# Kernel tuning notes

Measured on AMD Instinct MI355X. Metric: run time of the kernel, lower is better.

The kernel has to match this reference:

```python
import jax, jax.numpy as jnp
import numpy as np

DIMS = [2048, 2048, 2048, 2048, 1000]
BATCH = 1024
N_RELAX = 25
RELAX_LR = 0.3
N_LAYERS = len(DIMS) - 1  # 4 weight matrices, states indexed 0..4


def setup_inputs() -> dict:
    key = jax.random.key(0)
    ks = jax.random.split(key, N_LAYERS + 1)
    inp = {"x": jax.random.normal(ks[0], (BATCH, DIMS[0]), jnp.float32)}
    for i in range(N_LAYERS):
        scale = np.float32(np.sqrt(2.0 / DIMS[i]))
        inp[f"W{i}"] = jax.random.normal(ks[i + 1], (DIMS[i], DIMS[i + 1]), jnp.float32) * scale
    # biases[0] is never used in forward; biases[1..4] init to zeros as in torch code
    for l in range(1, N_LAYERS + 1):
        inp[f"b{l}"] = jnp.zeros((DIMS[l],), jnp.float32)
    return inp


def _rho(t):
    return jnp.clip(t, 0.0, 1.0)


def _relax(x, Ws, bs):
    # bs[l-1] corresponds to original biases[l] (state l's bias), l = 1..N_LAYERS
    # feedforward initialization pass
    states = [x]
    h = x
    for l in range(N_LAYERS):
        h = _rho(h @ Ws[l] + bs[l])
        states.append(h)

    # Gauss-Seidel sweep: states[l-1] already updated this iteration when l uses it
    def sweep(carry, _):
        full = [x] + list(carry)
        for l in range(1, N_LAYERS + 1):
            ds = -full[l] + bs[l - 1] + _rho(full[l - 1]) @ Ws[l - 1]
            if l < N_LAYERS:
                ds = ds + _rho(full[l + 1]) @ Ws[l].T
            full[l] = _rho(full[l] + RELAX_LR * ds)
        return tuple(full[1:]), None

    carry, _ = jax.lax.scan(sweep, tuple(states[1:]), None, length=N_RELAX)
    return carry


def reference(x, W0, W1, W2, W3, b1, b2, b3, b4):
    Ws = [W0, W1, W2, W3]
    bs = [b1, b2, b3, b4]
    states = _relax(x, Ws, bs)
    return states[-1]  # [BATCH, DIMS[-1]]
```

## Files before the change

### kernel.cpp

```cpp
#include <hip/hip_runtime.h>
#include <hip/hip_bf16.h>

typedef _Float16 fp16_t;
typedef _Float16 v8h __attribute__((ext_vector_type(8)));
typedef float    v4f __attribute__((ext_vector_type(4)));

#define RELAX_LR 0.3f

__device__ __forceinline__ void async_cp16(const void* g, void* l) {
    __builtin_amdgcn_global_load_lds(
        (const __attribute__((address_space(1))) void*)g,
        (__attribute__((address_space(3))) void*)l, 16, 0, 0);
}

__global__ __launch_bounds__(256, 2) void gemm_splitk_kernel(
    const fp16_t* __restrict__ A1, const fp16_t* __restrict__ B1t, int K1, int CK1, int nz1,
    const fp16_t* __restrict__ A2, const fp16_t* __restrict__ B2t, int K2s, int CK2,
    fp16_t* __restrict__ part, int Ntot)
{
    __shared__ __align__(16) fp16_t As[2][2][128][32];
    __shared__ __align__(16) fp16_t Bs[2][2][128][32];

    const int tid  = threadIdx.x;
    const int lane = tid & 63;
    const int w    = tid >> 6;
    const int wm   = w >> 1;
    const int wn   = w & 1;
    const int quad = lane >> 4;
    const int lrow = lane & 15;

    const int blk  = blockIdx.x;
    const int low3 = blk & 7;
    const int g    = blk >> 3;
    const int bm   = g & 7;
    const int c    = (g >> 3) * 8 + low3;
    int bn, z;
    if (Ntot == 2048) { bn = c >> 2; z = c & 3; }
    else              { bn = c >> 3; z = c & 7; }

    const fp16_t *A, *Bt; int stride, koff, CK;
    if (z < nz1) { A = A1; Bt = B1t; stride = K1;  CK = CK1; koff = z * CK1; }
    else         { A = A2; Bt = B2t; stride = K2s; CK = CK2; koff = (z - nz1) * CK2; }

    const int sr = lane >> 2;
    const int sc = (lane & 3) * 8;
    const fp16_t* ag = A  + (size_t)(bm * 128 + 32 * w + sr) * stride + koff + sc;
    const fp16_t* bg = Bt + (size_t)(bn * 128 + 32 * w + sr) * stride + koff + sc;
    const size_t st16 = (size_t)16 * stride;

    v4f acc[4][4] = {};
    const int iters = CK >> 6;

    auto stage = [&](int buf, int kb) {
        const fp16_t* a0 = ag + kb;
        const fp16_t* b0 = bg + kb;
        async_cp16(a0,             &As[buf][0][32 * w     ][0]);
        async_cp16(a0 + st16,      &As[buf][0][32 * w + 16][0]);
        async_cp16(a0 + 32,        &As[buf][1][32 * w     ][0]);
        async_cp16(a0 + 32 + st16, &As[buf][1][32 * w + 16][0]);
        async_cp16(b0,             &Bs[buf][0][32 * w     ][0]);
        async_cp16(b0 + st16,      &Bs[buf][0][32 * w + 16][0]);
        async_cp16(b0 + 32,        &Bs[buf][1][32 * w     ][0]);
        async_cp16(b0 + 32 + st16, &Bs[buf][1][32 * w + 16][0]);
    };

    stage(0, 0);

    for (int it = 0; it < iters; ++it) {
        __syncthreads();
        if (it + 1 < iters) stage((it + 1) & 1, (it + 1) * 64);
        const int cur = it & 1;
        #pragma unroll
        for (int h = 0; h < 2; ++h) {
            v8h af[4], bv[4];
            #pragma unroll
            for (int fm = 0; fm < 4; ++fm)
                af[fm] = *(const v8h*)&As[cur][h][wm * 64 + fm * 16 + lrow][quad * 8];
            #pragma unroll
            for (int fn = 0; fn < 4; ++fn)
                bv[fn] = *(const v8h*)&Bs[cur][h][wn * 64 + fn * 16 + lrow][quad * 8];
            #pragma unroll
            for (int fm = 0; fm < 4; ++fm)
                #pragma unroll
                for (int fn = 0; fn < 4; ++fn)
                    acc[fm][fn] = __builtin_amdgcn_mfma_f32_16x16x32_f16(
                        af[fm], bv[fn], acc[fm][fn], 0, 0, 0);
        }
    }

    fp16_t* po = part + (size_t)z * 1024 * Ntot;
    const int rowbase = bm * 128 + wm * 64 + quad * 4;
    const int colbase = bn * 128 + wn * 64;
    #pragma unroll
    for (int fn = 0; fn < 4; ++fn) {
        const int col = colbase + fn * 16 + lrow;
        #pragma unroll
        for (int fm = 0; fm < 4; ++fm) {
            const int row = rowbase + fm * 16;
            #pragma unroll
            for (int r = 0; r < 4; ++r)
                po[(size_t)(row + r) * Ntot + col] = (fp16_t)acc[fm][fn][r];
        }
    }
}

__global__ __launch_bounds__(256) void reduce_update_kernel(
    const fp16_t* __restrict__ part, int nz,
    const float* __restrict__ bias, const fp16_t* s_old,
    fp16_t* outb, int Ntot, int do_update, int total8)
{
    const int i = blockIdx.x * 256 + threadIdx.x;
    if (i >= total8) return;
    const size_t e = (size_t)i * 8;

    float v[8];
    {
        const v8h p0 = *(const v8h*)(part + e);
        #pragma unroll
        for (int j = 0; j < 8; ++j) v[j] = (float)p0[j];
    }
    for (int z = 1; z < nz; ++z) {
        const v8h p = *(const v8h*)(part + (size_t)z * 1024 * Ntot + e);
        #pragma unroll
        for (int j = 0; j < 8; ++j) v[j] += (float)p[j];
    }
    const int col = (int)e & (Ntot - 1);
    const float4 b0 = *(const float4*)(bias + col);
    const float4 b1 = *(const float4*)(bias + col + 4);
    v[0] += b0.x; v[1] += b0.y; v[2] += b0.z; v[3] += b0.w;
    v[4] += b1.x; v[5] += b1.y; v[6] += b1.z; v[7] += b1.w;
    if (do_update) {
        const v8h so = *(const v8h*)(s_old + e);
        #pragma unroll
        for (int j = 0; j < 8; ++j) {
            const float s = (float)so[j];
            v[j] = s + RELAX_LR * (v[j] - s);
        }
    }
    v8h h;
    #pragma unroll
    for (int j = 0; j < 8; ++j) h[j] = (fp16_t)fminf(fmaxf(v[j], 0.f), 1.f);
    *(v8h*)(outb + e) = h;
}

__global__ void conv_w_kernel(const float* __restrict__ W, int R, int C,
                              fp16_t* Wb, fp16_t* __restrict__ WbT,
                              int Rp, int Cp)
{
    __shared__ float t[32][33];
    const int tx = threadIdx.x & 31;
    const int ty = threadIdx.x >> 5;
    const int r0 = blockIdx.y * 32;
    const int c0 = blockIdx.x * 32;
    #pragma unroll
    for (int i = 0; i < 4; ++i) {
        const int r = r0 + ty + i * 8;
        const int c = c0 + tx;
        float v = 0.f;
        if (r < R && c < C) v = W[(size_t)r * C + c];
        t[ty + i * 8][tx] = v;
    }
    __syncthreads();
    if (Wb) {
        #pragma unroll
        for (int i = 0; i < 4; ++i) {
            const int r = r0 + ty + i * 8;
            const int c = c0 + tx;
            if (r < Rp && c < Cp) Wb[(size_t)r * Cp + c] = (fp16_t)t[ty + i * 8][tx];
        }
    }
    #pragma unroll
    for (int i = 0; i < 4; ++i) {
        const int cc = c0 + ty + i * 8;
        const int rr = r0 + tx;
        if (cc < Cp && rr < Rp) WbT[(size_t)cc * Rp + rr] = (fp16_t)t[tx][ty + i * 8];
    }
}

__global__ void conv_x_kernel(const float* __restrict__ x,
                              fp16_t* __restrict__ xb, fp16_t* __restrict__ rxb, int n)
{
    const int i = blockIdx.x * blockDim.x + threadIdx.x;
    if (i < n) {
        const float v = x[i];
        xb[i]  = (fp16_t)v;
        rxb[i] = (fp16_t)fminf(fmaxf(v, 0.f), 1.f);
    }
}

__global__ void pad_b4_kernel(const float* __restrict__ b4, float* __restrict__ b4p)
{
    const int i = blockIdx.x * blockDim.x + threadIdx.x;
    if (i < 1024) b4p[i] = (i < 1000) ? b4[i] : 0.f;
}

__global__ void out_copy_kernel(const fp16_t* __restrict__ s4b, float* __restrict__ out)
{
    const int i = blockIdx.x * blockDim.x + threadIdx.x;
    if (i < 1024 * 1000) {
        const int row = i / 1000;
        const int col = i - row * 1000;
        out[i] = (float)s4b[(size_t)row * 1024 + col];
    }
}

extern "C" void kernel_launch(void* const* d_in, const int* in_sizes, int n_in,
                              void* d_out, int out_size, void* d_ws, size_t ws_size,
                              hipStream_t stream)
{
    const float* x  = (const float*)d_in[0];
    const float* W0 = (const float*)d_in[1];
    const float* W1 = (const float*)d_in[2];
    const float* W2 = (const float*)d_in[3];
    const float* W3 = (const float*)d_in[4];
    const float* b1 = (const float*)d_in[5];
    const float* b2 = (const float*)d_in[6];
    const float* b3 = (const float*)d_in[7];
    const float* b4 = (const float*)d_in[8];
    float* out = (float*)d_out;

    char* p = (char*)d_ws;
    auto alloc = [&](size_t bytes) {
        char* q = p;
        p += (bytes + 255) & ~(size_t)255;
        return q;
    };

    fp16_t* xb   = (fp16_t*)alloc((size_t)1024 * 2048 * 2);
    fp16_t* rxb  = (fp16_t*)alloc((size_t)1024 * 2048 * 2);
    fp16_t* Wb1  = (fp16_t*)alloc((size_t)2048 * 2048 * 2);
    fp16_t* Wb2  = (fp16_t*)alloc((size_t)2048 * 2048 * 2);
    fp16_t* Wb3  = (fp16_t*)alloc((size_t)2048 * 1024 * 2);
    fp16_t* WbT0 = (fp16_t*)alloc((size_t)2048 * 2048 * 2);
    fp16_t* WbT1 = (fp16_t*)alloc((size_t)2048 * 2048 * 2);
    fp16_t* WbT2 = (fp16_t*)alloc((size_t)2048 * 2048 * 2);
    fp16_t* WbT3 = (fp16_t*)alloc((size_t)1024 * 2048 * 2);
    fp16_t* s1b  = (fp16_t*)alloc((size_t)1024 * 2048 * 2);
    fp16_t* s2b  = (fp16_t*)alloc((size_t)1024 * 2048 * 2);
    fp16_t* s3b  = (fp16_t*)alloc((size_t)1024 * 2048 * 2);
    fp16_t* s4b  = (fp16_t*)alloc((size_t)1024 * 1024 * 2);
    float*  b4p  = (float*)alloc(1024 * 4);
    fp16_t* part = (fp16_t*)alloc((size_t)4 * 1024 * 2048 * 2);
    (void)ws_size; (void)in_sizes; (void)n_in; (void)out_size;

    conv_x_kernel<<<(1024 * 2048 + 255) / 256, 256, 0, stream>>>(x, xb, rxb, 1024 * 2048);
    pad_b4_kernel<<<4, 256, 0, stream>>>(b4, b4p);
    conv_w_kernel<<<dim3(64, 64), 256, 0, stream>>>(W0, 2048, 2048, nullptr, WbT0, 2048, 2048);
    conv_w_kernel<<<dim3(64, 64), 256, 0, stream>>>(W1, 2048, 2048, Wb1, WbT1, 2048, 2048);
    conv_w_kernel<<<dim3(64, 64), 256, 0, stream>>>(W2, 2048, 2048, Wb2, WbT2, 2048, 2048);
    conv_w_kernel<<<dim3(32, 64), 256, 0, stream>>>(W3, 2048, 1000, Wb3, WbT3, 2048, 1024);

    const dim3 blk(256);
    const dim3 g512(512);
    const int t8_2048 = 1024 * 2048 / 8;
    const int t8_1024 = 1024 * 1024 / 8;
    const int rg2048 = t8_2048 / 256;
    const int rg1024 = t8_1024 / 256;

    gemm_splitk_kernel<<<g512, blk, 0, stream>>>(xb,  WbT0, 2048, 512, 4, nullptr, nullptr, 0, 0, part, 2048);
    reduce_update_kernel<<<rg2048, blk, 0, stream>>>(part, 4, b1, nullptr, s1b, 2048, 0, t8_2048);
    gemm_splitk_kernel<<<g512, blk, 0, stream>>>(s1b, WbT1, 2048, 512, 4, nullptr, nullptr, 0, 0, part, 2048);
    reduce_update_kernel<<<rg2048, blk, 0, stream>>>(part, 4, b2, nullptr, s2b, 2048, 0, t8_2048);
    gemm_splitk_kernel<<<g512, blk, 0, stream>>>(s2b, WbT2, 2048, 512, 4, nullptr, nullptr, 0, 0, part, 2048);
    reduce_update_kernel<<<rg2048, blk, 0, stream>>>(part, 4, b3, nullptr, s3b, 2048, 0, t8_2048);
    gemm_splitk_kernel<<<g512, blk, 0, stream>>>(s3b, WbT3, 2048, 256, 8, nullptr, nullptr, 0, 0, part, 1024);
    reduce_update_kernel<<<rg1024, blk, 0, stream>>>(part, 8, b4p, nullptr, s4b, 1024, 0, t8_1024);

    for (int it = 0; it < 25; ++it) {
        gemm_splitk_kernel<<<g512, blk, 0, stream>>>(rxb, WbT0, 2048, 1024, 2, s2b, Wb1, 2048, 1024, part, 2048);
        reduce_update_kernel<<<rg2048, blk, 0, stream>>>(part, 4, b1, s1b, s1b, 2048, 1, t8_2048);
        gemm_splitk_kernel<<<g512, blk, 0, stream>>>(s1b, WbT1, 2048, 1024, 2, s3b, Wb2, 2048, 1024, part, 2048);
        reduce_update_kernel<<<rg2048, blk, 0, stream>>>(part, 4, b2, s2b, s2b, 2048, 1, t8_2048);
        gemm_splitk_kernel<<<g512, blk, 0, stream>>>(s2b, WbT2, 2048, 1024, 2, s4b, Wb3, 1024, 512, part, 2048);
        reduce_update_kernel<<<rg2048, blk, 0, stream>>>(part, 4, b3, s3b, s3b, 2048, 1, t8_2048);
        gemm_splitk_kernel<<<g512, blk, 0, stream>>>(s3b, WbT3, 2048, 256, 8, nullptr, nullptr, 0, 0, part, 1024);
        reduce_update_kernel<<<rg1024, blk, 0, stream>>>(part, 8, b4p, s4b, s4b, 1024, 1, t8_1024);
    }

    out_copy_kernel<<<(1024 * 1000 + 255) / 256, 256, 0, stream>>>(s4b, out);
}
```

Measured before the change: 2.853 ms.

## Use two-wave GEMM blocks with 64x128 warp tiles and fuse output copy

The split-K GEMM now runs with 128 threads (2 waves) instead of 256, and each wave computes a 64x128 tile with 32 accumulators rather than 64x64. This raises MFMA work per LDS fragment load. Each wave stages a whole K-half of A and B. The final fp32 output is now written directly by the last reduce/update kernel, which removes the separate out_copy kernel. The trade-off is higher register pressure and fewer waves per block, which may reduce latency hiding.

```diff
diff --git a/kernel.cpp b/kernel.cpp
--- a/kernel.cpp
+++ b/kernel.cpp
@@ -13,7 +13,7 @@
         (__attribute__((address_space(3))) void*)l, 16, 0, 0);
 }
 
-__global__ __launch_bounds__(256, 2) void gemm_splitk_kernel(
+__global__ __launch_bounds__(128, 1) void gemm_splitk_kernel(
     const fp16_t* __restrict__ A1, const fp16_t* __restrict__ B1t, int K1, int CK1, int nz1,
     const fp16_t* __restrict__ A2, const fp16_t* __restrict__ B2t, int K2s, int CK2,
     fp16_t* __restrict__ part, int Ntot)
@@ -24,8 +24,6 @@
     const int tid  = threadIdx.x;
     const int lane = tid & 63;
     const int w    = tid >> 6;
-    const int wm   = w >> 1;
-    const int wn   = w & 1;
     const int quad = lane >> 4;
     const int lrow = lane & 15;
 
@@ -44,24 +42,21 @@
 
     const int sr = lane >> 2;
     const int sc = (lane & 3) * 8;
-    const fp16_t* ag = A  + (size_t)(bm * 128 + 32 * w + sr) * stride + koff + sc;
-    const fp16_t* bg = Bt + (size_t)(bn * 128 + 32 * w + sr) * stride + koff + sc;
+    const fp16_t* ag = A  + (size_t)(bm * 128 + sr) * stride + koff + sc + w * 32;
+    const fp16_t* bg = Bt + (size_t)(bn * 128 + sr) * stride + koff + sc + w * 32;
     const size_t st16 = (size_t)16 * stride;
 
-    v4f acc[4][4] = {};
+    v4f acc[4][8] = {};
     const int iters = CK >> 6;
 
     auto stage = [&](int buf, int kb) {
         const fp16_t* a0 = ag + kb;
         const fp16_t* b0 = bg + kb;
-        async_cp16(a0,             &As[buf][0][32 * w     ][0]);
-        async_cp16(a0 + st16,      &As[buf][0][32 * w + 16][0]);
-        async_cp16(a0 + 32,        &As[buf][1][32 * w     ][0]);
-        async_cp16(a0 + 32 + st16, &As[buf][1][32 * w + 16][0]);
-        async_cp16(b0,             &Bs[buf][0][32 * w     ][0]);
-        async_cp16(b0 + st16,      &Bs[buf][0][32 * w + 16][0]);
-        async_cp16(b0 + 32,        &Bs[buf][1][32 * w     ][0]);
-        async_cp16(b0 + 32 + st16, &Bs[buf][1][32 * w + 16][0]);
+        #pragma unroll
+        for (int gi = 0; gi < 8; ++gi) {
+            async_cp16(a0 + gi * st16, &As[buf][w][16 * gi][0]);
+            async_cp16(b0 + gi * st16, &Bs[buf][w][16 * gi][0]);
+        }
     };
 
     stage(0, 0);
@@ -72,27 +67,27 @@
         const int cur = it & 1;
         #pragma unroll
         for (int h = 0; h < 2; ++h) {
-            v8h af[4], bv[4];
+            v8h af[4], bv[8];
             #pragma unroll
             for (int fm = 0; fm < 4; ++fm)
-                af[fm] = *(const v8h*)&As[cur][h][wm * 64 + fm * 16 + lrow][quad * 8];
-            #pragma unroll
-            for (int fn = 0; fn < 4; ++fn)
-                bv[fn] = *(const v8h*)&Bs[cur][h][wn * 64 + fn * 16 + lrow][quad * 8];
+                af[fm] = *(const v8h*)&As[cur][h][w * 64 + fm * 16 + lrow][quad * 8];
+            #pragma unroll
+            for (int fn = 0; fn < 8; ++fn)
+                bv[fn] = *(const v8h*)&Bs[cur][h][fn * 16 + lrow][quad * 8];
             #pragma unroll
             for (int fm = 0; fm < 4; ++fm)
                 #pragma unroll
-                for (int fn = 0; fn < 4; ++fn)
+                for (int fn = 0; fn < 8; ++fn)
                     acc[fm][fn] = __builtin_amdgcn_mfma_f32_16x16x32_f16(
                         af[fm], bv[fn], acc[fm][fn], 0, 0, 0);
         }
     }
 
     fp16_t* po = part + (size_t)z * 1024 * Ntot;
-    const int rowbase = bm * 128 + wm * 64 + quad * 4;
-    const int colbase = bn * 128 + wn * 64;
-    #pragma unroll
-    for (int fn = 0; fn < 4; ++fn) {
+    const int rowbase = bm * 128 + w * 64 + quad * 4;
+    const int colbase = bn * 128;
+    #pragma unroll
+    for (int fn = 0; fn < 8; ++fn) {
         const int col = colbase + fn * 16 + lrow;
         #pragma unroll
         for (int fm = 0; fm < 4; ++fm) {
@@ -107,7 +102,8 @@
 __global__ __launch_bounds__(256) void reduce_update_kernel(
     const fp16_t* __restrict__ part, int nz,
     const float* __restrict__ bias, const fp16_t* s_old,
-    fp16_t* outb, int Ntot, int do_update, int total8)
+    fp16_t* outb, int Ntot, int do_update, int total8,
+    float* __restrict__ finout)
 {
     const int i = blockIdx.x * 256 + threadIdx.x;
     if (i >= total8) return;
@@ -137,10 +133,21 @@
             v[j] = s + RELAX_LR * (v[j] - s);
         }
     }
+    #pragma unroll
+    for (int j = 0; j < 8; ++j) v[j] = fminf(fmaxf(v[j], 0.f), 1.f);
     v8h h;
     #pragma unroll
-    for (int j = 0; j < 8; ++j) h[j] = (fp16_t)fminf(fmaxf(v[j], 0.f), 1.f);
+    for (int j = 0; j < 8; ++j) h[j] = (fp16_t)v[j];
     *(v8h*)(outb + e) = h;
+
+    if (finout && col < 1000) {
+        const int row = (int)(e >> 10);
+        float* o = finout + (size_t)row * 1000 + col;
+        float4 o0 = {v[0], v[1], v[2], v[3]};
+        float4 o1 = {v[4], v[5], v[6], v[7]};
+        *(float4*)o       = o0;
+        *(float4*)(o + 4) = o1;
+    }
 }
 
 __global__ void conv_w_kernel(const float* __restrict__ W, int R, int C,
@@ -192,16 +199,6 @@
 {
     const int i = blockIdx.x * blockDim.x + threadIdx.x;
     if (i < 1024) b4p[i] = (i < 1000) ? b4[i] : 0.f;
-}
-
-__global__ void out_copy_kernel(const fp16_t* __restrict__ s4b, float* __restrict__ out)
-{
-    const int i = blockIdx.x * blockDim.x + threadIdx.x;
-    if (i < 1024 * 1000) {
-        const int row = i / 1000;
-        const int col = i - row * 1000;
-        out[i] = (float)s4b[(size_t)row * 1024 + col];
-    }
 }
 
 extern "C" void kernel_launch(void* const* d_in, const int* in_sizes, int n_in,
@@ -250,32 +247,32 @@
     conv_w_kernel<<<dim3(64, 64), 256, 0, stream>>>(W2, 2048, 2048, Wb2, WbT2, 2048, 2048);
     conv_w_kernel<<<dim3(32, 64), 256, 0, stream>>>(W3, 2048, 1000, Wb3, WbT3, 2048, 1024);
 
-    const dim3 blk(256);
+    const dim3 gblk(128);
     const dim3 g512(512);
+    const dim3 rblk(256);
     const int t8_2048 = 1024 * 2048 / 8;
     const int t8_1024 = 1024 * 1024 / 8;
     const int rg2048 = t8_2048 / 256;
     const int rg1024 = t8_1024 / 256;
 
-    gemm_splitk_kernel<<<g512, blk, 0, stream>>>(xb,  WbT0, 2048, 512, 4, nullptr, nullptr, 0, 0, part, 2048);
-    reduce_update_kernel<<<rg2048, blk, 0, stream>>>(part, 4, b1, nullptr, s1b, 2048, 0, t8_2048);
-    gemm_splitk_kernel<<<g512, blk, 0, stream>>>(s1b, WbT1, 2048, 512, 4, nullptr, nullptr, 0, 0, part, 2048);
-    reduce_update_kernel<<<rg2048, blk, 0, stream>>>(part, 4, b2, nullptr, s2b, 2048, 0, t8_2048);
-    gemm_splitk_kernel<<<g512, blk, 0, stream>>>(s2b, WbT2, 2048, 512, 4, nullptr, nullptr, 0, 0, part, 2048);
-    reduce_update_kernel<<<rg2048, blk, 0, stream>>>(part, 4, b3, nullptr, s3b, 2048, 0, t8_2048);
-    gemm_splitk_kernel<<<g512, blk, 0, stream>>>(s3b, WbT3, 2048, 256, 8, nullptr, nullptr, 0, 0, part, 1024);
-    reduce_update_kernel<<<rg1024, blk, 0, stream>>>(part, 8, b4p, nullptr, s4b, 1024, 0, t8_1024);
+    gemm_splitk_kernel<<<g512, gblk, 0, stream>>>(xb,  WbT0, 2048, 512, 4, nullptr, nullptr, 0, 0, part, 2048);
+    reduce_update_kernel<<<rg2048, rblk, 0, stream>>>(part, 4, b1, nullptr, s1b, 2048, 0, t8_2048, nullptr);
+    gemm_splitk_kernel<<<g512, gblk, 0, stream>>>(s1b, WbT1, 2048, 512, 4, nullptr, nullptr, 0, 0, part, 2048);
+    reduce_update_kernel<<<rg2048, rblk, 0, stream>>>(part, 4, b2, nullptr, s2b, 2048, 0, t8_2048, nullptr);
+    gemm_splitk_kernel<<<g512, gblk, 0, stream>>>(s2b, WbT2, 2048, 512, 4, nullptr, nullptr, 0, 0, part, 2048);
+    reduce_update_kernel<<<rg2048, rblk, 0, stream>>>(part, 4, b3, nullptr, s3b, 2048, 0, t8_2048, nullptr);
+    gemm_splitk_kernel<<<g512, gblk, 0, stream>>>(s3b, WbT3, 2048, 256, 8, nullptr, nullptr, 0, 0, part, 1024);
+    reduce_update_kernel<<<rg1024, rblk, 0, stream>>>(part, 8, b4p, nullptr, s4b, 1024, 0, t8_1024, nullptr);
 
     for (int it = 0; it < 25; ++it) {
-        gemm_splitk_kernel<<<g512, blk, 0, stream>>>(rxb, WbT0, 2048, 1024, 2, s2b, Wb1, 2048, 1024, part, 2048);
-        reduce_update_kernel<<<rg2048, blk, 0, stream>>>(part, 4, b1, s1b, s1b, 2048, 1, t8_2048);
-        gemm_splitk_kernel<<<g512, blk, 0, stream>>>(s1b, WbT1, 2048, 1024, 2, s3b, Wb2, 2048, 1024, part, 2048);
-        reduce_update_kernel<<<rg2048, blk, 0, stream>>>(part, 4, b2, s2b, s2b, 2048, 1, t8_2048);
-        gemm_splitk_kernel<<<g512, blk, 0, stream>>>(s2b, WbT2, 2048, 1024, 2, s4b, Wb3, 1024, 512, part, 2048);
-        reduce_update_kernel<<<rg2048, blk, 0, stream>>>(part, 4, b3, s3b, s3b, 2048, 1, t8_2048);
-        gemm_splitk_kernel<<<g512, blk, 0, stream>>>(s3b, WbT3, 2048, 256, 8, nullptr, nullptr, 0, 0, part, 1024);
-        reduce_update_kernel<<<rg1024, blk, 0, stream>>>(part, 8, b4p, s4b, s4b, 1024, 1, t8_1024);
-    }
-
-    out_copy_kernel<<<(1024 * 1000 + 255) / 256, 256, 0, stream>>>(s4b, out);
-}
+        gemm_splitk_kernel<<<g512, gblk, 0, stream>>>(rxb, WbT0, 2048, 1024, 2, s2b, Wb1, 2048, 1024, part, 2048);
+        reduce_update_kernel<<<rg2048, rblk, 0, stream>>>(part, 4, b1, s1b, s1b, 2048, 1, t8_2048, nullptr);
+        gemm_splitk_kernel<<<g512, gblk, 0, stream>>>(s1b, WbT1, 2048, 1024, 2, s3b, Wb2, 2048, 1024, part, 2048);
+        reduce_update_kernel<<<rg2048, rblk, 0, stream>>>(part, 4, b2, s2b, s2b, 2048, 1, t8_2048, nullptr);
+        gemm_splitk_kernel<<<g512, gblk, 0, stream>>>(s2b, WbT2, 2048, 1024, 2, s4b, Wb3, 1024, 512, part, 2048);
+        reduce_update_kernel<<<rg2048, rblk, 0, stream>>>(part, 4, b3, s3b, s3b, 2048, 1, t8_2048, nullptr);
+        gemm_splitk_kernel<<<g512, gblk, 0, stream>>>(s3b, WbT3, 2048, 256, 8, nullptr, nullptr, 0, 0, part, 1024);
+        reduce_update_kernel<<<rg1024, rblk, 0, stream>>>(part, 8, b4p, s4b, s4b, 1024, 1, t8_1024,
+                                                          (it == 24) ? out : nullptr);
+    }
+}
```

After: 3.389 ms. 18.8% more time.

## Hoist loop-invariant rho(x)@W0 term out of relaxation loop

Applied to the files above, without the earlier changes.

The layer-1 update term rho(x)@W0 + b1 never changes across the 25 relaxation sweeps, so it is now computed once into an fp32 buffer and added in the reduce step. Each iteration's first GEMM shrinks from K=4096 (two concatenated operands) to K=2048. The final fp32 output is also written directly by the last layer-4 reduce, which removes the separate output copy kernel. This costs an extra 8 MB fp32 buffer that is read every iteration.

```diff
diff --git a/kernel.cpp b/kernel.cpp
--- a/kernel.cpp
+++ b/kernel.cpp
@@ -106,8 +106,9 @@
 
 __global__ __launch_bounds__(256) void reduce_update_kernel(
     const fp16_t* __restrict__ part, int nz,
-    const float* __restrict__ bias, const fp16_t* s_old,
-    fp16_t* outb, int Ntot, int do_update, int total8)
+    const float* __restrict__ bias, const float* __restrict__ extra,
+    const fp16_t* s_old, fp16_t* outb,
+    int Ntot, int do_update, int total8, float* __restrict__ finout)
 {
     const int i = blockIdx.x * 256 + threadIdx.x;
     if (i >= total8) return;
@@ -125,22 +126,70 @@
         for (int j = 0; j < 8; ++j) v[j] += (float)p[j];
     }
     const int col = (int)e & (Ntot - 1);
+    if (extra) {
+        const float4 e0 = *(const float4*)(extra + e);
+        const float4 e1 = *(const float4*)(extra + e + 4);
+        v[0] += e0.x; v[1] += e0.y; v[2] += e0.z; v[3] += e0.w;
+        v[4] += e1.x; v[5] += e1.y; v[6] += e1.z; v[7] += e1.w;
+    } else {
+        const float4 b0 = *(const float4*)(bias + col);
+        const float4 b1 = *(const float4*)(bias + col + 4);
+        v[0] += b0.x; v[1] += b0.y; v[2] += b0.z; v[3] += b0.w;
+        v[4] += b1.x; v[5] += b1.y; v[6] += b1.z; v[7] += b1.w;
+    }
+    if (do_update) {
+        const v8h so = *(const v8h*)(s_old + e);
+        #pragma unroll
+        for (int j = 0; j < 8; ++j) {
+            const float s = (float)so[j];
+            v[j] = s + RELAX_LR * (v[j] - s);
+        }
+    }
+    #pragma unroll
+    for (int j = 0; j < 8; ++j) v[j] = fminf(fmaxf(v[j], 0.f), 1.f);
+    v8h h;
+    #pragma unroll
+    for (int j = 0; j < 8; ++j) h[j] = (fp16_t)v[j];
+    *(v8h*)(outb + e) = h;
+
+    if (finout && col < 1000) {
+        const int row = (int)(e >> 10);
+        float* o = finout + (size_t)row * 1000 + col;
+        float4 o0 = {v[0], v[1], v[2], v[3]};
+        float4 o1 = {v[4], v[5], v[6], v[7]};
+        *(float4*)o       = o0;
+        *(float4*)(o + 4) = o1;
+    }
+}
+
+__global__ __launch_bounds__(256) void makec1_kernel(
+    const fp16_t* __restrict__ part, const float* __restrict__ bias,
+    float* __restrict__ c1f, int total8)
+{
+    const int i = blockIdx.x * 256 + threadIdx.x;
+    if (i >= total8) return;
+    const size_t e = (size_t)i * 8;
+    float v[8];
+    {
+        const v8h p0 = *(const v8h*)(part + e);
+        #pragma unroll
+        for (int j = 0; j < 8; ++j) v[j] = (float)p0[j];
+    }
+    #pragma unroll
+    for (int z = 1; z < 4; ++z) {
+        const v8h p = *(const v8h*)(part + (size_t)z * 1024 * 2048 + e);
+        #pragma unroll
+        for (int j = 0; j < 8; ++j) v[j] += (float)p[j];
+    }
+    const int col = (int)e & 2047;
     const float4 b0 = *(const float4*)(bias + col);
     const float4 b1 = *(const float4*)(bias + col + 4);
     v[0] += b0.x; v[1] += b0.y; v[2] += b0.z; v[3] += b0.w;
     v[4] += b1.x; v[5] += b1.y; v[6] += b1.z; v[7] += b1.w;
-    if (do_update) {
-        const v8h so = *(const v8h*)(s_old + e);
-        #pragma unroll
-        for (int j = 0; j < 8; ++j) {
-            const float s = (float)so[j];
-            v[j] = s + RELAX_LR * (v[j] - s);
-        }
-    }
-    v8h h;
-    #pragma unroll
-    for (int j = 0; j < 8; ++j) h[j] = (fp16_t)fminf(fmaxf(v[j], 0.f), 1.f);
-    *(v8h*)(outb + e) = h;
+    float4 o0 = {v[0], v[1], v[2], v[3]};
+    float4 o1 = {v[4], v[5], v[6], v[7]};
+    *(float4*)(c1f + e)     = o0;
+    *(float4*)(c1f + e + 4) = o1;
 }
 
 __global__ void conv_w_kernel(const float* __restrict__ W, int R, int C,
@@ -192,16 +241,6 @@
 {
     const int i = blockIdx.x * blockDim.x + threadIdx.x;
     if (i < 1024) b4p[i] = (i < 1000) ? b4[i] : 0.f;
-}
-
-__global__ void out_copy_kernel(const fp16_t* __restrict__ s4b, float* __restrict__ out)
-{
-    const int i = blockIdx.x * blockDim.x + threadIdx.x;
-    if (i < 1024 * 1000) {
-        const int row = i / 1000;
-        const int col = i - row * 1000;
-        out[i] = (float)s4b[(size_t)row * 1024 + col];
-    }
 }
 
 extern "C" void kernel_launch(void* const* d_in, const int* in_sizes, int n_in,
@@ -240,6 +279,7 @@
     fp16_t* s3b  = (fp16_t*)alloc((size_t)1024 * 2048 * 2);
     fp16_t* s4b  = (fp16_t*)alloc((size_t)1024 * 1024 * 2);
     float*  b4p  = (float*)alloc(1024 * 4);
+    float*  c1f  = (float*)alloc((size_t)1024 * 2048 * 4);
     fp16_t* part = (fp16_t*)alloc((size_t)4 * 1024 * 2048 * 2);
     (void)ws_size; (void)in_sizes; (void)n_in; (void)out_size;
 
@@ -257,25 +297,27 @@
     const int rg2048 = t8_2048 / 256;
     const int rg1024 = t8_1024 / 256;
 
+    gemm_splitk_kernel<<<g512, blk, 0, stream>>>(rxb, WbT0, 2048, 512, 4, nullptr, nullptr, 0, 0, part, 2048);
+    makec1_kernel<<<rg2048, blk, 0, stream>>>(part, b1, c1f, t8_2048);
+
     gemm_splitk_kernel<<<g512, blk, 0, stream>>>(xb,  WbT0, 2048, 512, 4, nullptr, nullptr, 0, 0, part, 2048);
-    reduce_update_kernel<<<rg2048, blk, 0, stream>>>(part, 4, b1, nullptr, s1b, 2048, 0, t8_2048);
+    reduce_update_kernel<<<rg2048, blk, 0, stream>>>(part, 4, b1, nullptr, nullptr, s1b, 2048, 0, t8_2048, nullptr);
     gemm_splitk_kernel<<<g512, blk, 0, stream>>>(s1b, WbT1, 2048, 512, 4, nullptr, nullptr, 0, 0, part, 2048);
-    reduce_update_kernel<<<rg2048, blk, 0, stream>>>(part, 4, b2, nullptr, s2b, 2048, 0, t8_2048);
+    reduce_update_kernel<<<rg2048, blk, 0, stream>>>(part, 4, b2, nullptr, nullptr, s2b, 2048, 0, t8_2048, nullptr);
     gemm_splitk_kernel<<<g512, blk, 0, stream>>>(s2b, WbT2, 2048, 512, 4, nullptr, nullptr, 0, 0, part, 2048);
-    reduce_update_kernel<<<rg2048, blk, 0, stream>>>(part, 4, b3, nullptr, s3b, 2048, 0, t8_2048);
+    reduce_update_kernel<<<rg2048, blk, 0, stream>>>(part, 4, b3, nullptr, nullptr, s3b, 2048, 0, t8_2048, nullptr);
     gemm_splitk_kernel<<<g512, blk, 0, stream>>>(s3b, WbT3, 2048, 256, 8, nullptr, nullptr, 0, 0, part, 1024);
-    reduce_update_kernel<<<rg1024, blk, 0, stream>>>(part, 8, b4p, nullptr, s4b, 1024, 0, t8_1024);
+    reduce_update_kernel<<<rg1024, blk, 0, stream>>>(part, 8, b4p, nullptr, nullptr, s4b, 1024, 0, t8_1024, nullptr);
 
     for (int it = 0; it < 25; ++it) {
-        gemm_splitk_kernel<<<g512, blk, 0, stream>>>(rxb, WbT0, 2048, 1024, 2, s2b, Wb1, 2048, 1024, part, 2048);
-        reduce_update_kernel<<<rg2048, blk, 0, stream>>>(part, 4, b1, s1b, s1b, 2048, 1, t8_2048);
+        gemm_splitk_kernel<<<g512, blk, 0, stream>>>(s2b, Wb1, 2048, 512, 4, nullptr, nullptr, 0, 0, part, 2048);
+        reduce_update_kernel<<<rg2048, blk, 0, stream>>>(part, 4, nullptr, c1f, s1b, s1b, 2048, 1, t8_2048, nullptr);
         gemm_splitk_kernel<<<g512, blk, 0, stream>>>(s1b, WbT1, 2048, 1024, 2, s3b, Wb2, 2048, 1024, part, 2048);
-        reduce_update_kernel<<<rg2048, blk, 0, stream>>>(part, 4, b2, s2b, s2b, 2048, 1, t8_2048);
+        reduce_update_kernel<<<rg2048, blk, 0, stream>>>(part, 4, b2, nullptr, s2b, s2b, 2048, 1, t8_2048, nullptr);
         gemm_splitk_kernel<<<g512, blk, 0, stream>>>(s2b, WbT2, 2048, 1024, 2, s4b, Wb3, 1024, 512, part, 2048);
-        reduce_update_kernel<<<rg2048, blk, 0, stream>>>(part, 4, b3, s3b, s3b, 2048, 1, t8_2048);
+        reduce_update_kernel<<<rg2048, blk, 0, stream>>>(part, 4, b3, nullptr, s3b, s3b, 2048, 1, t8_2048, nullptr);
         gemm_splitk_kernel<<<g512, blk, 0, stream>>>(s3b, WbT3, 2048, 256, 8, nullptr, nullptr, 0, 0, part, 1024);
-        reduce_update_kernel<<<rg1024, blk, 0, stream>>>(part, 8, b4p, s4b, s4b, 1024, 1, t8_1024);
-    }
-
-    out_copy_kernel<<<(1024 * 1000 + 255) / 256, 256, 0, stream>>>(s4b, out);
-}
+        reduce_update_kernel<<<rg1024, blk, 0, stream>>>(part, 8, b4p, nullptr, s4b, s4b, 1024, 1, t8_1024,
+                                                         (it == 24) ? out : nullptr);
+    }
+}
```

New measurement: 2.757 ms. 3.4% less time.
